# Performance work log

Hardware: AMD Instinct MI355X
Metric: run time of the kernel (lower is better)

Reference implementation:

```python
import jax, jax.numpy as jnp
import numpy as np

N = 100000
K = 4
E = 1600000
EPS = 1e-5


def gcn_conv(x, src, dst, W, b):
    # PyG GCNConv with improved=True: self-loop weight 2, symmetric norm.
    h = x @ W  # [N, out]
    ones = jnp.ones(src.shape, dtype=x.dtype)
    deg = jax.ops.segment_sum(ones, dst, num_segments=N) + 2.0  # improved self-loop adds 2
    dis = jax.lax.rsqrt(deg)
    coef = dis[src] * dis[dst]  # [E]
    agg = jax.ops.segment_sum(h[src] * coef[:, None], dst, num_segments=N)
    agg = agg + (2.0 * dis * dis)[:, None] * h  # self-loop contribution (weight 2)
    return agg + b


def expert_forward(flatten, src, dst, W1, b1, g, bt, W2, b2):
    x = gcn_conv(flatten, src, dst, W1, b1)
    x = jax.nn.relu(x)
    # BatchNorm1d(track_running_stats=False): batch statistics, biased var
    mu = jnp.mean(x, axis=0)
    var = jnp.mean(jnp.square(x - mu), axis=0)
    x = (x - mu) * jax.lax.rsqrt(var + EPS) * g + bt
    return gcn_conv(x, src, dst, W2, b2)  # [N, 2] logits


def setup_inputs() -> dict:
    key = jax.random.key(0)
    ks = jax.random.split(key, 8)
    flatten = jax.random.normal(ks[0], (N, 256), dtype=jnp.float32)
    moe_features = jax.random.normal(ks[1], (N, 256), dtype=jnp.float32)
    edge_index = jax.random.randint(ks[2], (K, 2, E), 0, N, dtype=jnp.int32)
    W1 = jax.random.normal(ks[3], (K, 256, 64), dtype=jnp.float32) * 0.05
    b1 = jnp.zeros((K, 64), dtype=jnp.float32)
    gamma = jnp.ones((K, 64), dtype=jnp.float32)
    beta = jnp.zeros((K, 64), dtype=jnp.float32)
    W2 = jax.random.normal(ks[4], (K, 64, 2), dtype=jnp.float32) * 0.1
    b2 = jnp.zeros((K, 2), dtype=jnp.float32)
    Wg = jax.random.normal(ks[5], (256, K), dtype=jnp.float32) * 0.05
    bg = jnp.zeros((K,), dtype=jnp.float32)
    return {"flatten": flatten, "moe_features": moe_features, "edge_index": edge_index,
            "W1": W1, "b1": b1, "gamma": gamma, "beta": beta, "W2": W2, "b2": b2,
            "Wg": Wg, "bg": bg}


def reference(flatten, moe_features, edge_index, W1, b1, gamma, beta, W2, b2, Wg, bg):
    src = edge_index[:, 0, :]
    dst = edge_index[:, 1, :]
    # run all experts batched via vmap (flatten shared)
    logits = jax.vmap(expert_forward, in_axes=(None, 0, 0, 0, 0, 0, 0, 0, 0))(
        flatten, src, dst, W1, b1, gamma, beta, W2, b2)  # [K, N, 2]
    logp = jax.nn.log_softmax(logits, axis=-1)
    probs = jax.nn.softmax(logits, axis=-1)
    weights = jax.nn.softmax(moe_features @ Wg + bg, axis=1)  # [N, K]
    # results_concat[:, c] = sum_k weights[:, k] * logp[k, :, c]
    results_concat = jnp.einsum('nk,knc->nc', weights, logp)
    results_probs_concat = jnp.einsum('nk,knc->nc', weights, probs)
    return results_concat, results_probs_concat
```

## Files before the change

kernel.cpp:

```cpp
#include <hip/hip_runtime.h>
#include <math.h>

#define NN 100000
#define KEXP 4
#define EE 1600000
#define EPSV 1e-5f
#define BSHIFT 9
#define BSIZE 512
#define NBUCK 196
#define PCHUNK 4096
#define PG ((EE + PCHUNK - 1) / PCHUNK)
#define SLOTS 64
#define STAGECAP 12288

typedef __attribute__((ext_vector_type(8))) short bfrag8;
typedef __attribute__((ext_vector_type(16))) float facc16;

__device__ __forceinline__ unsigned short f2bf(float f) {
    unsigned u = __float_as_uint(f);
    return (unsigned short)((u + 0x7fff + ((u >> 16) & 1)) >> 16);
}
__device__ __forceinline__ float bf_lo(unsigned u) { return __uint_as_float(u << 16); }
__device__ __forceinline__ float bf_hi(unsigned u) { return __uint_as_float(u & 0xffff0000u); }

__global__ __launch_bounds__(256) void hist_pass(const int* __restrict__ edge,
                                                 int* __restrict__ blockhist, int E) {
    int k = blockIdx.y, bx = blockIdx.x;
    const int* dp = edge + (size_t)k * 2 * E + E;
    __shared__ int hist[NBUCK];
    for (int i = threadIdx.x; i < NBUCK; i += 256) hist[i] = 0;
    __syncthreads();
    int cb = bx * PCHUNK, ce = cb + PCHUNK;
    if (ce > E) ce = E;
    for (int e = cb + (int)threadIdx.x; e < ce; e += 256)
        atomicAdd(&hist[dp[e] >> BSHIFT], 1);
    __syncthreads();
    for (int i = threadIdx.x; i < NBUCK; i += 256)
        blockhist[((size_t)k * PG + bx) * NBUCK + i] = hist[i];
}

__global__ __launch_bounds__(256) void scan_pass(int* __restrict__ blockhist,
                                                 int* __restrict__ bbase,
                                                 int* __restrict__ rowptr,
                                                 int n, int E) {
    int k = blockIdx.x;
    int t = threadIdx.x;
    int running = 0;
    if (t < NBUCK) {
        for (int j = 0; j < PG; j++) {
            size_t idx = ((size_t)k * PG + j) * NBUCK + t;
            int v = blockhist[idx];
            blockhist[idx] = running;
            running += v;
        }
    }
    __shared__ int sd[256];
    sd[t] = (t < NBUCK) ? running : 0;
    __syncthreads();
    for (int o = 1; o < 256; o <<= 1) {
        int x = (t >= o) ? sd[t - o] : 0;
        __syncthreads();
        sd[t] += x;
        __syncthreads();
    }
    if (t < NBUCK) bbase[k * (NBUCK + 1) + t] = sd[t] - running;
    if (t == 0) {
        bbase[k * (NBUCK + 1) + NBUCK] = E;
        rowptr[(size_t)k * (n + 1) + n] = E;
    }
}

__global__ __launch_bounds__(256) void partition_pass(const int* __restrict__ edge,
                                                      const int* __restrict__ blockhist,
                                                      const int* __restrict__ bbase,
                                                      unsigned* __restrict__ bstream,
                                                      int E) {
    int k = blockIdx.y, bx = blockIdx.x;
    int t = threadIdx.x;
    __shared__ int hist[NBUCK];
    __shared__ int lofs[NBUCK + 1];
    __shared__ int gbase[NBUCK];
    __shared__ int tmp[256];
    __shared__ unsigned stage[PCHUNK];
    for (int i = t; i < NBUCK; i += 256) {
        hist[i] = 0;
        gbase[i] = bbase[k * (NBUCK + 1) + i] + blockhist[((size_t)k * PG + bx) * NBUCK + i];
    }
    __syncthreads();
    const int* sp = edge + (size_t)k * 2 * E;
    const int* dp = sp + E;
    int cb = bx * PCHUNK, ce = cb + PCHUNK;
    if (ce > E) ce = E;
    int cnt = ce - cb;
    for (int e = cb + t; e < ce; e += 256)
        atomicAdd(&hist[dp[e] >> BSHIFT], 1);
    __syncthreads();
    int v = (t < NBUCK) ? hist[t] : 0;
    tmp[t] = v;
    __syncthreads();
    for (int o = 1; o < 256; o <<= 1) {
        int x = (t >= o) ? tmp[t - o] : 0;
        __syncthreads();
        tmp[t] += x;
        __syncthreads();
    }
    if (t < NBUCK) { lofs[t] = tmp[t] - v; hist[t] = tmp[t] - v; }
    if (t == 0) lofs[NBUCK] = cnt;
    __syncthreads();
    for (int e = cb + t; e < ce; e += 256) {
        int s = sp[e];
        int d = dp[e];
        int r = atomicAdd(&hist[d >> BSHIFT], 1);
        stage[r] = ((unsigned)(d & (BSIZE - 1)) << 17) | (unsigned)s;
    }
    __syncthreads();
    unsigned* bs = bstream + (size_t)k * E;
    for (int i = t; i < cnt; i += 256) {
        int lo = 0, hi = NBUCK;
        while (hi - lo > 1) {
            int mid = (lo + hi) >> 1;
            if (lofs[mid] <= i) lo = mid; else hi = mid;
        }
        bs[gbase[lo] + (i - lofs[lo])] = stage[i];
    }
}

__global__ __launch_bounds__(256) void bucket_build(const int* __restrict__ bbase,
                                                    const unsigned* __restrict__ bstream,
                                                    int* __restrict__ rowptr,
                                                    float* __restrict__ dis,
                                                    int* __restrict__ adj,
                                                    int n, int E) {
    int k = blockIdx.y;
    int b = blockIdx.x;
    int nb = b << BSHIFT;
    int t = threadIdx.x;
    __shared__ int hist[BSIZE];
    __shared__ int curx[BSIZE];
    __shared__ int tmp[256];
    __shared__ int stage[STAGECAP];
    hist[t] = 0;
    hist[t + 256] = 0;
    __syncthreads();
    int beg = bbase[k * (NBUCK + 1) + b];
    int end = bbase[k * (NBUCK + 1) + b + 1];
    int cnt = end - beg;
    const unsigned* bs = bstream + (size_t)k * E;
    for (int p = beg + t; p < end; p += 256) {
        atomicAdd(&hist[bs[p] >> 17], 1);
    }
    __syncthreads();
    int a0 = hist[2 * t], a1 = hist[2 * t + 1];
    tmp[t] = a0 + a1;
    __syncthreads();
    for (int o = 1; o < 256; o <<= 1) {
        int x = (t >= o) ? tmp[t - o] : 0;
        __syncthreads();
        tmp[t] += x;
        __syncthreads();
    }
    int ex = tmp[t] - (a0 + a1);
    int l0 = ex;
    int l1 = ex + a0;
    curx[2 * t] = l0;
    curx[2 * t + 1] = l1;
    int* rp = rowptr + (size_t)k * (n + 1);
    float* dk = dis + (size_t)k * n;
    int node0 = nb + 2 * t, node1 = nb + 2 * t + 1;
    if (node0 < n) { rp[node0] = beg + l0; dk[node0] = rsqrtf((float)a0 + 2.0f); }
    if (node1 < n) { rp[node1] = beg + l1; dk[node1] = rsqrtf((float)a1 + 2.0f); }
    __syncthreads();
    int* aj = adj + (size_t)k * E;
    for (int p = beg + t; p < end; p += 256) {
        unsigned pk = bs[p];
        int pos = atomicAdd(&curx[pk >> 17], 1);
        int sv = (int)(pk & 0x1FFFFu);
        if (pos < STAGECAP) stage[pos] = sv;
        else aj[beg + pos] = sv;
    }
    __syncthreads();
    int lim = cnt < STAGECAP ? cnt : STAGECAP;
    int head = (4 - (beg & 3)) & 3;
    if (head > lim) head = lim;
    if (t < head) aj[beg + t] = stage[t];
    int nv = (lim - head) >> 2;
    for (int i = t; i < nv; i += 256) {
        int s4 = head + 4 * i;
        uint4 v = make_uint4((unsigned)stage[s4], (unsigned)stage[s4 + 1],
                             (unsigned)stage[s4 + 2], (unsigned)stage[s4 + 3]);
        *(uint4*)&aj[beg + s4] = v;
    }
    int tail0 = head + 4 * nv;
    for (int i = tail0 + t; i < lim; i += 256) aj[beg + i] = stage[i];
}

__global__ __launch_bounds__(256) void a2bf_kernel(const float* __restrict__ A,
                                                   unsigned short* __restrict__ abf,
                                                   int n4) {
    int i = blockIdx.x * 256 + threadIdx.x;
    if (i >= n4) return;
    float4 v = ((const float4*)A)[i];
    ushort4 o;
    o.x = f2bf(v.x); o.y = f2bf(v.y); o.z = f2bf(v.z); o.w = f2bf(v.w);
    ((ushort4*)abf)[i] = o;
}

__global__ __launch_bounds__(256) void w2bf_kernel(const float* __restrict__ W1,
                                                   unsigned short* __restrict__ Wt) {
    int k = blockIdx.x;
    for (int idx = threadIdx.x; idx < 64 * 256; idx += 256) {
        int c = idx >> 8;
        int kk = idx & 255;
        Wt[(size_t)k * 64 * 256 + c * 256 + kk] = f2bf(W1[(size_t)k * 256 * 64 + kk * 64 + c]);
    }
}

__global__ __launch_bounds__(256) void gemm1_mfma(
    const unsigned short* __restrict__ abf,
    const unsigned short* __restrict__ Wt,
    const float* __restrict__ dk,
    unsigned short* __restrict__ phbf,
    int M) {
    __shared__ __align__(16) unsigned short As[64][72];
    __shared__ __align__(16) unsigned short Bs[64][72];
    int t = threadIdx.x;
    int row0 = blockIdx.x * 64;
    int wid = t >> 6, lane = t & 63;
    int qr = wid >> 1, qc = wid & 1;
    facc16 acc;
    for (int i = 0; i < 16; i++) acc[i] = 0.f;

    for (int kc = 0; kc < 256; kc += 64) {
        for (int i = 0; i < 2; i++) {
            int fid = t + i * 256;
            int r = fid >> 3;
            int o = (fid & 7) * 8;
            int row = row0 + r;
            uint4 v = make_uint4(0u, 0u, 0u, 0u);
            if (row < M) v = *(const uint4*)&abf[(size_t)row * 256 + kc + o];
            *(uint4*)&As[r][o] = v;
        }
        for (int i = 0; i < 2; i++) {
            int fid = t + i * 256;
            int c = fid >> 3;
            int o = (fid & 7) * 8;
            uint4 v = *(const uint4*)&Wt[(size_t)c * 256 + kc + o];
            *(uint4*)&Bs[c][o] = v;
        }
        __syncthreads();
        int arow = qr * 32 + (lane & 31);
        int bcol = qc * 32 + (lane & 31);
        int ko = (lane >> 5) * 8;
        for (int kk = 0; kk < 64; kk += 16) {
            bfrag8 a = *(const bfrag8*)&As[arow][kk + ko];
            bfrag8 b = *(const bfrag8*)&Bs[bcol][kk + ko];
            acc = __builtin_amdgcn_mfma_f32_32x32x16_bf16(a, b, acc, 0, 0, 0);
        }
        __syncthreads();
    }
    int col = qc * 32 + (lane & 31);
    for (int i = 0; i < 16; i++) {
        int rl = (i & 3) + 8 * (i >> 2) + 4 * (lane >> 5);
        int row = row0 + qr * 32 + rl;
        if (row < M) phbf[(size_t)row * 64 + col] = f2bf(dk[row] * acc[i]);
    }
}

__global__ __launch_bounds__(256) void gemm1_fp32(
    const float* __restrict__ A, const float* __restrict__ W,
    const float* __restrict__ dk,
    unsigned short* __restrict__ phbf, int M) {
    __shared__ __align__(16) float As[64][65];
    __shared__ __align__(16) float Ws[64][68];
    int t = threadIdx.x;
    int row0 = blockIdx.x * 64;
    int tr = t >> 4;
    int tc = t & 15;
    float acc[4][4] = {{0.f}};
    for (int kc = 0; kc < 256; kc += 64) {
        for (int i = 0; i < 4; i++) {
            int fid = t + i * 256;
            int r = fid >> 4;
            int c4 = (fid & 15) << 2;
            int row = row0 + r;
            float4 v = make_float4(0.f, 0.f, 0.f, 0.f);
            if (row < M) v = *(const float4*)&A[(size_t)row * 256 + kc + c4];
            As[r][c4] = v.x; As[r][c4 + 1] = v.y; As[r][c4 + 2] = v.z; As[r][c4 + 3] = v.w;
        }
        for (int i = 0; i < 4; i++) {
            int fid = t + i * 256;
            int r = fid >> 4;
            int c4 = (fid & 15) << 2;
            float4 v = *(const float4*)&W[(size_t)(kc + r) * 64 + c4];
            *(float4*)&Ws[r][c4] = v;
        }
        __syncthreads();
        for (int kk = 0; kk < 64; kk++) {
            float a0 = As[tr * 4 + 0][kk];
            float a1 = As[tr * 4 + 1][kk];
            float a2 = As[tr * 4 + 2][kk];
            float a3 = As[tr * 4 + 3][kk];
            float4 w = *(const float4*)&Ws[kk][tc * 4];
            acc[0][0] += a0 * w.x; acc[0][1] += a0 * w.y; acc[0][2] += a0 * w.z; acc[0][3] += a0 * w.w;
            acc[1][0] += a1 * w.x; acc[1][1] += a1 * w.y; acc[1][2] += a1 * w.z; acc[1][3] += a1 * w.w;
            acc[2][0] += a2 * w.x; acc[2][1] += a2 * w.y; acc[2][2] += a2 * w.z; acc[2][3] += a2 * w.w;
            acc[3][0] += a3 * w.x; acc[3][1] += a3 * w.y; acc[3][2] += a3 * w.z; acc[3][3] += a3 * w.w;
        }
        __syncthreads();
    }
    for (int i = 0; i < 4; i++) {
        int row = row0 + tr * 4 + i;
        if (row >= M) continue;
        float dn = dk[row];
        ushort4 o;
        o.x = f2bf(dn * acc[i][0]); o.y = f2bf(dn * acc[i][1]);
        o.z = f2bf(dn * acc[i][2]); o.w = f2bf(dn * acc[i][3]);
        *(ushort4*)&phbf[(size_t)row * 64 + 4 * tc] = o;
    }
}

__global__ __launch_bounds__(256) void gather1(const int* __restrict__ rowptr,
                                               const int* __restrict__ adj,
                                               const float* __restrict__ dis,
                                               const unsigned short* __restrict__ phbf,
                                               const float* __restrict__ b1,
                                               float* __restrict__ x,
                                               float* __restrict__ accum, int n) {
    __shared__ float ls[4][64];
    __shared__ float lq[4][64];
    ((float*)ls)[threadIdx.x] = 0.f;
    ((float*)lq)[threadIdx.x] = 0.f;
    __syncthreads();
    int w = threadIdx.x >> 6;
    int node = blockIdx.x * 4 + w;
    int lane = threadIdx.x & 63;
    int g = lane >> 4;
    int q = lane & 15;
    if (node < n) {
        int beg = rowptr[node], end = rowptr[node + 1];
        float a0 = 0.f, a1 = 0.f, a2 = 0.f, a3 = 0.f;
        float c0 = 0.f, c1 = 0.f, c2 = 0.f, c3 = 0.f;
        int j = beg;
        for (; j + 8 <= end; j += 8) {
            int s0 = adj[j + g];
            int s1 = adj[j + 4 + g];
            uint2 u0 = *(const uint2*)&phbf[(size_t)s0 * 64 + 4 * q];
            uint2 u1 = *(const uint2*)&phbf[(size_t)s1 * 64 + 4 * q];
            a0 += bf_lo(u0.x); a1 += bf_hi(u0.x);
            a2 += bf_lo(u0.y); a3 += bf_hi(u0.y);
            c0 += bf_lo(u1.x); c1 += bf_hi(u1.x);
            c2 += bf_lo(u1.y); c3 += bf_hi(u1.y);
        }
        for (; j < end; j += 4) {
            int jj = j + g;
            if (jj < end) {
                int s = adj[jj];
                uint2 u = *(const uint2*)&phbf[(size_t)s * 64 + 4 * q];
                a0 += bf_lo(u.x); a1 += bf_hi(u.x);
                a2 += bf_lo(u.y); a3 += bf_hi(u.y);
            }
        }
        a0 += c0; a1 += c1; a2 += c2; a3 += c3;
        a0 += __shfl_xor(a0, 16); a1 += __shfl_xor(a1, 16);
        a2 += __shfl_xor(a2, 16); a3 += __shfl_xor(a3, 16);
        a0 += __shfl_xor(a0, 32); a1 += __shfl_xor(a1, 32);
        a2 += __shfl_xor(a2, 32); a3 += __shfl_xor(a3, 32);
        if (g == 0) {
            float dn = dis[node];
            uint2 us = *(const uint2*)&phbf[(size_t)node * 64 + 4 * q];
            float4 bv = *(const float4*)&b1[4 * q];
            float v0 = dn * (a0 + 2.f * bf_lo(us.x)) + bv.x;
            float v1 = dn * (a1 + 2.f * bf_hi(us.x)) + bv.y;
            float v2 = dn * (a2 + 2.f * bf_lo(us.y)) + bv.z;
            float v3 = dn * (a3 + 2.f * bf_hi(us.y)) + bv.w;
            v0 = fmaxf(v0, 0.f); v1 = fmaxf(v1, 0.f);
            v2 = fmaxf(v2, 0.f); v3 = fmaxf(v3, 0.f);
            *(float4*)&x[(size_t)node * 64 + 4 * q] = make_float4(v0, v1, v2, v3);
            *(float4*)&ls[w][4 * q] = make_float4(v0, v1, v2, v3);
            *(float4*)&lq[w][4 * q] = make_float4(v0 * v0, v1 * v1, v2 * v2, v3 * v3);
        }
    }
    __syncthreads();
    if (threadIdx.x < 64) {
        int c = threadIdx.x;
        float S = ls[0][c] + ls[1][c] + ls[2][c] + ls[3][c];
        float Q = lq[0][c] + lq[1][c] + lq[2][c] + lq[3][c];
        float* slot = accum + (size_t)(blockIdx.x & (SLOTS - 1)) * 128;
        unsafeAtomicAdd(&slot[c], S);
        unsafeAtomicAdd(&slot[64 + c], Q);
    }
}

__global__ __launch_bounds__(256) void bn_gemm2(const float* __restrict__ x,
                                                const float* __restrict__ accum,
                                                const float* __restrict__ g,
                                                const float* __restrict__ bt,
                                                const float* __restrict__ W2,
                                                const float* __restrict__ dk,
                                                float* __restrict__ ph, int M) {
    __shared__ float a_s[64], b_s[64];
    int t = threadIdx.x;
    if (t < 64) {
        float S = 0.f, Q = 0.f;
        for (int s = 0; s < SLOTS; s++) {
            S += accum[(size_t)s * 128 + t];
            Q += accum[(size_t)s * 128 + 64 + t];
        }
        float mu = S / (float)M;
        float var = Q / (float)M - mu * mu;
        float istdg = rsqrtf(var + EPSV) * g[t];
        a_s[t] = istdg;
        b_s[t] = bt[t] - mu * istdg;
    }
    __syncthreads();
    int w = t >> 6;
    int c = t & 63;
    float a = a_s[c], b = b_s[c];
    float w20 = W2[c * 2], w21 = W2[c * 2 + 1];
    for (int node = blockIdx.x * 4 + w; node < M; node += gridDim.x * 4) {
        float v = x[(size_t)node * 64 + c] * a + b;
        float p0 = v * w20;
        float p1 = v * w21;
        for (int off = 32; off; off >>= 1) {
            p0 += __shfl_down(p0, off);
            p1 += __shfl_down(p1, off);
        }
        if (c == 0) {
            float dn = dk[node];
            *(float2*)&ph[(size_t)node * 2] = make_float2(dn * p0, dn * p1);
        }
    }
}

__global__ __launch_bounds__(256) void gather2_all(const int* __restrict__ rowptr,
                                                   const int* __restrict__ adj,
                                                   const float* __restrict__ dis,
                                                   const float* __restrict__ phall,
                                                   const float* __restrict__ b2,
                                                   float* __restrict__ agg2,
                                                   int n, int E) {
    int B = blockIdx.x;
    int k = (B & 7) >> 1;
    int jb = ((B >> 3) << 1) | (B & 1);
    int node = jb * 256 + (int)threadIdx.x;
    if (node >= n) return;
    const int* rp = rowptr + (size_t)k * (n + 1);
    const int* aj = adj + (size_t)k * E;
    const float* ph = phall + (size_t)k * n * 2;
    float dn = dis[(size_t)k * n + node];
    int beg = rp[node], end = rp[node + 1];
    float a0 = 0.f, a1 = 0.f;
    int j = beg;
    for (; j + 2 <= end; j += 2) {
        int s0 = aj[j], s1 = aj[j + 1];
        float2 v0 = *(const float2*)&ph[(size_t)s0 * 2];
        float2 v1 = *(const float2*)&ph[(size_t)s1 * 2];
        a0 += v0.x + v1.x;
        a1 += v0.y + v1.y;
    }
    if (j < end) {
        int s0 = aj[j];
        float2 v0 = *(const float2*)&ph[(size_t)s0 * 2];
        a0 += v0.x;
        a1 += v0.y;
    }
    float2 pn = *(const float2*)&ph[(size_t)node * 2];
    float2 o;
    o.x = dn * (a0 + 2.f * pn.x) + b2[k * 2];
    o.y = dn * (a1 + 2.f * pn.y) + b2[k * 2 + 1];
    *(float2*)&agg2[((size_t)k * n + node) * 2] = o;
}

__global__ __launch_bounds__(256) void gate_kernel(const float* __restrict__ moe,
                                                   const float* __restrict__ Wg,
                                                   const float* __restrict__ bg,
                                                   float* __restrict__ wbuf, int M) {
    int n = (int)((blockIdx.x * (size_t)blockDim.x + threadIdx.x) >> 6);
    int lane = threadIdx.x & 63;
    if (n >= M) return;
    float4 mf = *(const float4*)&moe[(size_t)n * 256 + lane * 4];
    const float* wr = &Wg[lane * 16];
    float a0 = mf.x * wr[0] + mf.y * wr[4] + mf.z * wr[8] + mf.w * wr[12];
    float a1 = mf.x * wr[1] + mf.y * wr[5] + mf.z * wr[9] + mf.w * wr[13];
    float a2 = mf.x * wr[2] + mf.y * wr[6] + mf.z * wr[10] + mf.w * wr[14];
    float a3 = mf.x * wr[3] + mf.y * wr[7] + mf.z * wr[11] + mf.w * wr[15];
    for (int mask = 1; mask < 64; mask <<= 1) {
        a0 += __shfl_xor(a0, mask);
        a1 += __shfl_xor(a1, mask);
        a2 += __shfl_xor(a2, mask);
        a3 += __shfl_xor(a3, mask);
    }
    if (lane == 0) {
        float g0 = a0 + bg[0], g1 = a1 + bg[1], g2 = a2 + bg[2], g3 = a3 + bg[3];
        float m = fmaxf(fmaxf(g0, g1), fmaxf(g2, g3));
        float w0 = expf(g0 - m), w1 = expf(g1 - m), w2 = expf(g2 - m), w3 = expf(g3 - m);
        float inv = 1.f / (w0 + w1 + w2 + w3);
        *(float4*)&wbuf[(size_t)n * 4] =
            make_float4(w0 * inv, w1 * inv, w2 * inv, w3 * inv);
    }
}

__global__ __launch_bounds__(256) void mix_kernel(const float* __restrict__ wbuf,
                                                  const float* __restrict__ agg2,
                                                  float* __restrict__ out, int M) {
    int n = blockIdx.x * 256 + threadIdx.x;
    if (n >= M) return;
    float4 wv = *(const float4*)&wbuf[(size_t)n * 4];
    float wk[4] = {wv.x, wv.y, wv.z, wv.w};
    float o0 = 0.f, o1 = 0.f, q0 = 0.f, q1 = 0.f;
    for (int kk = 0; kk < 4; kk++) {
        float2 l = *(const float2*)&agg2[((size_t)kk * M + n) * 2];
        float mm = fmaxf(l.x, l.y);
        float lse = mm + logf(expf(l.x - mm) + expf(l.y - mm));
        float lp0 = l.x - lse, lp1 = l.y - lse;
        o0 += wk[kk] * lp0; o1 += wk[kk] * lp1;
        q0 += wk[kk] * expf(lp0); q1 += wk[kk] * expf(lp1);
    }
    *(float2*)&out[(size_t)n * 2] = make_float2(o0, o1);
    *(float2*)&out[(size_t)2 * M + n * 2] = make_float2(q0, q1);
}

extern "C" void kernel_launch(void* const* d_in, const int* in_sizes, int n_in,
                              void* d_out, int out_size, void* d_ws, size_t ws_size,
                              hipStream_t stream) {
    const float* flatten = (const float*)d_in[0];
    const float* moe     = (const float*)d_in[1];
    const int*   edge    = (const int*)d_in[2];
    const float* W1      = (const float*)d_in[3];
    const float* b1      = (const float*)d_in[4];
    const float* gamma   = (const float*)d_in[5];
    const float* beta    = (const float*)d_in[6];
    const float* W2      = (const float*)d_in[7];
    const float* b2      = (const float*)d_in[8];
    const float* Wg      = (const float*)d_in[9];
    const float* bg      = (const float*)d_in[10];
    float* out = (float*)d_out;

    const int N = NN, E = EE, K = KEXP;

    char* ws = (char*)d_ws;
    size_t off = 0;
    auto alloc = [&](size_t bytes) -> void* {
        void* p = (void*)(ws + off);
        off += (bytes + 255) & ~(size_t)255;
        return p;
    };
    int*   rowptr    = (int*)alloc((size_t)K * (N + 1) * 4);
    float* dis       = (float*)alloc((size_t)K * N * 4);
    int*   blockhist = (int*)alloc((size_t)K * PG * NBUCK * 4);
    int*   bbase     = (int*)alloc((size_t)K * (NBUCK + 1) * 4);
    int*   adj       = (int*)alloc((size_t)K * E * 4);
    unsigned short* hbf = (unsigned short*)alloc((size_t)N * 64 * 2);
    float* x         = (float*)alloc((size_t)N * 64 * 4);
    float* h2all     = (float*)alloc((size_t)K * N * 2 * 4);
    float* agg2      = (float*)alloc((size_t)K * N * 2 * 4);
    float* accum     = (float*)alloc((size_t)K * SLOTS * 128 * 4);
    float* wbuf      = (float*)alloc((size_t)N * 4 * 4);
    size_t base_need = off;
    unsigned short* abf = (unsigned short*)alloc((size_t)N * 256 * 2);
    unsigned short* Wt  = (unsigned short*)alloc((size_t)K * 64 * 256 * 2);
    size_t mfma_need = off;
    (void)in_sizes; (void)n_in; (void)out_size; (void)base_need;
    bool use_mfma = (ws_size >= mfma_need);

    unsigned* bstream = (unsigned*)hbf;

    hipMemsetAsync(accum, 0, (size_t)K * SLOTS * 128 * 4, stream);
    hist_pass<<<dim3(PG, K), 256, 0, stream>>>(edge, blockhist, E);
    scan_pass<<<K, 256, 0, stream>>>(blockhist, bbase, rowptr, N, E);
    partition_pass<<<dim3(PG, K), 256, 0, stream>>>(edge, blockhist, bbase, bstream, E);
    bucket_build<<<dim3(NBUCK, K), 256, 0, stream>>>(bbase, bstream, rowptr, dis, adj, N, E);

    if (use_mfma) {
        a2bf_kernel<<<(N * 256 / 4 + 255) / 256, 256, 0, stream>>>(flatten, abf, N * 256 / 4);
        w2bf_kernel<<<K, 256, 0, stream>>>(W1, Wt);
    }

    gate_kernel<<<(int)(((size_t)N * 64 + 255) / 256), 256, 0, stream>>>(
        moe, Wg, bg, wbuf, N);

    for (int k = 0; k < K; k++) {
        const int* rp = rowptr + (size_t)k * (N + 1);
        const int* aj = adj + (size_t)k * E;
        const float* dk = dis + (size_t)k * N;
        float* ak = accum + (size_t)k * SLOTS * 128;
        if (use_mfma) {
            gemm1_mfma<<<(N + 63) / 64, 256, 0, stream>>>(
                abf, Wt + (size_t)k * 64 * 256, dk, hbf, N);
        } else {
            gemm1_fp32<<<(N + 63) / 64, 256, 0, stream>>>(
                flatten, W1 + (size_t)k * 256 * 64, dk, hbf, N);
        }
        gather1<<<(N + 3) / 4, 256, 0, stream>>>(
            rp, aj, dk, hbf, b1 + (size_t)k * 64, x, ak, N);
        bn_gemm2<<<1024, 256, 0, stream>>>(
            x, ak, gamma + (size_t)k * 64, beta + (size_t)k * 64,
            W2 + (size_t)k * 128, dk, h2all + (size_t)k * N * 2, N);
    }
    gather2_all<<<1568, 256, 0, stream>>>(
        rowptr, adj, dis, h2all, b2, agg2, N, E);
    mix_kernel<<<(N + 255) / 256, 256, 0, stream>>>(wbuf, agg2, out, N);
}
```

Measured before the change: 834.9 us.

## Batch all experts into single launches per stage and rework gate kernel

When the workspace is large enough, all four experts now run together: the per-expert loop of three launches each is replaced by one GEMM1, one gather1 and one BN+GEMM2 launch that cover every expert via the grid y dimension or an index decode that interleaves experts across blocks. This removes launch gaps and lets the per-expert stages fill the GPU concurrently, at the cost of K-fold larger intermediate buffers (bf16 h and fp32 x for all experts). The gate kernel also changes from one wavefront per row with shuffle reductions to one thread per row, with Wg staged in shared memory. The old sequential path is kept as a fallback when the workspace is small.

```diff
diff --git a/kernel.cpp b/kernel.cpp
--- a/kernel.cpp
+++ b/kernel.cpp
@@ -215,12 +215,16 @@
     }
 }
 
-__global__ __launch_bounds__(256) void gemm1_mfma(
+__global__ __launch_bounds__(256) void gemm1_mfma_all(
     const unsigned short* __restrict__ abf,
-    const unsigned short* __restrict__ Wt,
-    const float* __restrict__ dk,
-    unsigned short* __restrict__ phbf,
+    const unsigned short* __restrict__ Wtall,
+    const float* __restrict__ dis,
+    unsigned short* __restrict__ phall,
     int M) {
+    int k = blockIdx.y;
+    const unsigned short* Wt = Wtall + (size_t)k * 64 * 256;
+    const float* dk = dis + (size_t)k * M;
+    unsigned short* phbf = phall + (size_t)k * M * 64;
     __shared__ __align__(16) unsigned short As[64][72];
     __shared__ __align__(16) unsigned short Bs[64][72];
     int t = threadIdx.x;
@@ -266,10 +270,14 @@
     }
 }
 
-__global__ __launch_bounds__(256) void gemm1_fp32(
-    const float* __restrict__ A, const float* __restrict__ W,
-    const float* __restrict__ dk,
-    unsigned short* __restrict__ phbf, int M) {
+__global__ __launch_bounds__(256) void gemm1_fp32_all(
+    const float* __restrict__ A, const float* __restrict__ W1,
+    const float* __restrict__ dis,
+    unsigned short* __restrict__ phall, int M) {
+    int k = blockIdx.y;
+    const float* W = W1 + (size_t)k * 256 * 64;
+    const float* dk = dis + (size_t)k * M;
+    unsigned short* phbf = phall + (size_t)k * M * 64;
     __shared__ __align__(16) float As[64][65];
     __shared__ __align__(16) float Ws[64][68];
     int t = threadIdx.x;
@@ -319,31 +327,47 @@
     }
 }
 
-__global__ __launch_bounds__(256) void gather1(const int* __restrict__ rowptr,
-                                               const int* __restrict__ adj,
-                                               const float* __restrict__ dis,
-                                               const unsigned short* __restrict__ phbf,
-                                               const float* __restrict__ b1,
-                                               float* __restrict__ x,
-                                               float* __restrict__ accum, int n) {
+__global__ __launch_bounds__(256) void gather1_all(const int* __restrict__ rowptr,
+                                                   const int* __restrict__ adj,
+                                                   const float* __restrict__ dis,
+                                                   const unsigned short* __restrict__ phall,
+                                                   const float* __restrict__ b1all,
+                                                   float* __restrict__ xall,
+                                                   float* __restrict__ accum,
+                                                   int n, int E, int merged) {
+    int B = blockIdx.x;
+    int k, nb4;
+    if (merged) {
+        k = (B >> 1) & 3;
+        nb4 = (((B >> 3) << 1) | (B & 1));
+    } else {
+        k = 0;
+        nb4 = B;
+    }
+    const int* rp = rowptr + (size_t)k * (n + 1);
+    const int* aj = adj + (size_t)k * E;
+    const unsigned short* phbf = phall + (size_t)k * n * 64;
+    const float* b1 = b1all + (size_t)k * 64;
+    float* x = xall + (size_t)k * n * 64;
+
     __shared__ float ls[4][64];
     __shared__ float lq[4][64];
     ((float*)ls)[threadIdx.x] = 0.f;
     ((float*)lq)[threadIdx.x] = 0.f;
     __syncthreads();
     int w = threadIdx.x >> 6;
-    int node = blockIdx.x * 4 + w;
+    int node = nb4 * 4 + w;
     int lane = threadIdx.x & 63;
     int g = lane >> 4;
     int q = lane & 15;
     if (node < n) {
-        int beg = rowptr[node], end = rowptr[node + 1];
+        int beg = rp[node], end = rp[node + 1];
         float a0 = 0.f, a1 = 0.f, a2 = 0.f, a3 = 0.f;
         float c0 = 0.f, c1 = 0.f, c2 = 0.f, c3 = 0.f;
         int j = beg;
         for (; j + 8 <= end; j += 8) {
-            int s0 = adj[j + g];
-            int s1 = adj[j + 4 + g];
+            int s0 = aj[j + g];
+            int s1 = aj[j + 4 + g];
             uint2 u0 = *(const uint2*)&phbf[(size_t)s0 * 64 + 4 * q];
             uint2 u1 = *(const uint2*)&phbf[(size_t)s1 * 64 + 4 * q];
             a0 += bf_lo(u0.x); a1 += bf_hi(u0.x);
@@ -354,7 +378,7 @@
         for (; j < end; j += 4) {
             int jj = j + g;
             if (jj < end) {
-                int s = adj[jj];
+                int s = aj[jj];
                 uint2 u = *(const uint2*)&phbf[(size_t)s * 64 + 4 * q];
                 a0 += bf_lo(u.x); a1 += bf_hi(u.x);
                 a2 += bf_lo(u.y); a3 += bf_hi(u.y);
@@ -366,7 +390,7 @@
         a0 += __shfl_xor(a0, 32); a1 += __shfl_xor(a1, 32);
         a2 += __shfl_xor(a2, 32); a3 += __shfl_xor(a3, 32);
         if (g == 0) {
-            float dn = dis[node];
+            float dn = dis[(size_t)k * n + node];
             uint2 us = *(const uint2*)&phbf[(size_t)node * 64 + 4 * q];
             float4 bv = *(const float4*)&b1[4 * q];
             float v0 = dn * (a0 + 2.f * bf_lo(us.x)) + bv.x;
@@ -385,26 +409,34 @@
         int c = threadIdx.x;
         float S = ls[0][c] + ls[1][c] + ls[2][c] + ls[3][c];
         float Q = lq[0][c] + lq[1][c] + lq[2][c] + lq[3][c];
-        float* slot = accum + (size_t)(blockIdx.x & (SLOTS - 1)) * 128;
+        float* slot = accum + (size_t)k * SLOTS * 128 + (size_t)(nb4 & (SLOTS - 1)) * 128;
         unsafeAtomicAdd(&slot[c], S);
         unsafeAtomicAdd(&slot[64 + c], Q);
     }
 }
 
-__global__ __launch_bounds__(256) void bn_gemm2(const float* __restrict__ x,
-                                                const float* __restrict__ accum,
-                                                const float* __restrict__ g,
-                                                const float* __restrict__ bt,
-                                                const float* __restrict__ W2,
-                                                const float* __restrict__ dk,
-                                                float* __restrict__ ph, int M) {
+__global__ __launch_bounds__(256) void bn_gemm2_all(const float* __restrict__ xall,
+                                                    const float* __restrict__ accum,
+                                                    const float* __restrict__ gall,
+                                                    const float* __restrict__ btall,
+                                                    const float* __restrict__ W2all,
+                                                    const float* __restrict__ dis,
+                                                    float* __restrict__ h2all, int M) {
+    int k = blockIdx.y;
+    const float* x = xall + (size_t)k * M * 64;
+    const float* acb = accum + (size_t)k * SLOTS * 128;
+    const float* g = gall + (size_t)k * 64;
+    const float* bt = btall + (size_t)k * 64;
+    const float* W2 = W2all + (size_t)k * 128;
+    const float* dk = dis + (size_t)k * M;
+    float* ph = h2all + (size_t)k * M * 2;
     __shared__ float a_s[64], b_s[64];
     int t = threadIdx.x;
     if (t < 64) {
         float S = 0.f, Q = 0.f;
         for (int s = 0; s < SLOTS; s++) {
-            S += accum[(size_t)s * 128 + t];
-            Q += accum[(size_t)s * 128 + 64 + t];
+            S += acb[(size_t)s * 128 + t];
+            Q += acb[(size_t)s * 128 + 64 + t];
         }
         float mu = S / (float)M;
         float var = Q / (float)M - mu * mu;
@@ -475,29 +507,27 @@
                                                    const float* __restrict__ Wg,
                                                    const float* __restrict__ bg,
                                                    float* __restrict__ wbuf, int M) {
-    int n = (int)((blockIdx.x * (size_t)blockDim.x + threadIdx.x) >> 6);
-    int lane = threadIdx.x & 63;
+    __shared__ float wg_s[1024];
+    for (int i = threadIdx.x; i < 1024; i += 256) wg_s[i] = Wg[i];
+    __syncthreads();
+    int n = blockIdx.x * 256 + threadIdx.x;
     if (n >= M) return;
-    float4 mf = *(const float4*)&moe[(size_t)n * 256 + lane * 4];
-    const float* wr = &Wg[lane * 16];
-    float a0 = mf.x * wr[0] + mf.y * wr[4] + mf.z * wr[8] + mf.w * wr[12];
-    float a1 = mf.x * wr[1] + mf.y * wr[5] + mf.z * wr[9] + mf.w * wr[13];
-    float a2 = mf.x * wr[2] + mf.y * wr[6] + mf.z * wr[10] + mf.w * wr[14];
-    float a3 = mf.x * wr[3] + mf.y * wr[7] + mf.z * wr[11] + mf.w * wr[15];
-    for (int mask = 1; mask < 64; mask <<= 1) {
-        a0 += __shfl_xor(a0, mask);
-        a1 += __shfl_xor(a1, mask);
-        a2 += __shfl_xor(a2, mask);
-        a3 += __shfl_xor(a3, mask);
-    }
-    if (lane == 0) {
-        float g0 = a0 + bg[0], g1 = a1 + bg[1], g2 = a2 + bg[2], g3 = a3 + bg[3];
-        float m = fmaxf(fmaxf(g0, g1), fmaxf(g2, g3));
-        float w0 = expf(g0 - m), w1 = expf(g1 - m), w2 = expf(g2 - m), w3 = expf(g3 - m);
-        float inv = 1.f / (w0 + w1 + w2 + w3);
-        *(float4*)&wbuf[(size_t)n * 4] =
-            make_float4(w0 * inv, w1 * inv, w2 * inv, w3 * inv);
-    }
+    const float4* row = (const float4*)&moe[(size_t)n * 256];
+    float a0 = 0.f, a1 = 0.f, a2 = 0.f, a3 = 0.f;
+    #pragma unroll 8
+    for (int j = 0; j < 64; j++) {
+        float4 v = row[j];
+        const float* wj = &wg_s[j * 16];
+        a0 += v.x * wj[0] + v.y * wj[4] + v.z * wj[8]  + v.w * wj[12];
+        a1 += v.x * wj[1] + v.y * wj[5] + v.z * wj[9]  + v.w * wj[13];
+        a2 += v.x * wj[2] + v.y * wj[6] + v.z * wj[10] + v.w * wj[14];
+        a3 += v.x * wj[3] + v.y * wj[7] + v.z * wj[11] + v.w * wj[15];
+    }
+    float g0 = a0 + bg[0], g1 = a1 + bg[1], g2 = a2 + bg[2], g3 = a3 + bg[3];
+    float m = fmaxf(fmaxf(g0, g1), fmaxf(g2, g3));
+    float w0 = expf(g0 - m), w1 = expf(g1 - m), w2 = expf(g2 - m), w3 = expf(g3 - m);
+    float inv = 1.f / (w0 + w1 + w2 + w3);
+    *(float4*)&wbuf[(size_t)n * 4] = make_float4(w0 * inv, w1 * inv, w2 * inv, w3 * inv);
 }
 
 __global__ __launch_bounds__(256) void mix_kernel(const float* __restrict__ wbuf,
@@ -550,20 +580,29 @@
     int*   blockhist = (int*)alloc((size_t)K * PG * NBUCK * 4);
     int*   bbase     = (int*)alloc((size_t)K * (NBUCK + 1) * 4);
     int*   adj       = (int*)alloc((size_t)K * E * 4);
-    unsigned short* hbf = (unsigned short*)alloc((size_t)N * 64 * 2);
-    float* x         = (float*)alloc((size_t)N * 64 * 4);
     float* h2all     = (float*)alloc((size_t)K * N * 2 * 4);
     float* agg2      = (float*)alloc((size_t)K * N * 2 * 4);
     float* accum     = (float*)alloc((size_t)K * SLOTS * 128 * 4);
     float* wbuf      = (float*)alloc((size_t)N * 4 * 4);
-    size_t base_need = off;
-    unsigned short* abf = (unsigned short*)alloc((size_t)N * 256 * 2);
-    unsigned short* Wt  = (unsigned short*)alloc((size_t)K * 64 * 256 * 2);
-    size_t mfma_need = off;
-    (void)in_sizes; (void)n_in; (void)out_size; (void)base_need;
-    bool use_mfma = (ws_size >= mfma_need);
-
-    unsigned* bstream = (unsigned*)hbf;
+    unsigned short* Wt = (unsigned short*)alloc((size_t)K * 64 * 256 * 2);
+    size_t common_end = off;
+
+    unsigned short* phallA = (unsigned short*)alloc((size_t)K * N * 64 * 2);
+    float* xallA = (float*)alloc((size_t)K * N * 64 * 4);
+    size_t merged_need = off;
+
+    off = common_end;
+    unsigned short* hbfB = (unsigned short*)alloc((size_t)N * 64 * 2);
+    float* xB = (float*)alloc((size_t)N * 64 * 4);
+    size_t fb_base_need = off;
+    unsigned short* abfB = (unsigned short*)alloc((size_t)N * 256 * 2);
+    size_t fb_mfma_need = off;
+    (void)in_sizes; (void)n_in; (void)out_size; (void)fb_base_need;
+
+    bool merged = (ws_size >= merged_need);
+    bool fb_mfma = (ws_size >= fb_mfma_need);
+
+    unsigned* bstream = merged ? (unsigned*)phallA : (unsigned*)hbfB;
 
     hipMemsetAsync(accum, 0, (size_t)K * SLOTS * 128 * 4, stream);
     hist_pass<<<dim3(PG, K), 256, 0, stream>>>(edge, blockhist, E);
@@ -571,31 +610,40 @@
     partition_pass<<<dim3(PG, K), 256, 0, stream>>>(edge, blockhist, bbase, bstream, E);
     bucket_build<<<dim3(NBUCK, K), 256, 0, stream>>>(bbase, bstream, rowptr, dis, adj, N, E);
 
-    if (use_mfma) {
+    gate_kernel<<<(N + 255) / 256, 256, 0, stream>>>(moe, Wg, bg, wbuf, N);
+
+    if (merged) {
+        unsigned short* abf = (unsigned short*)xallA;
         a2bf_kernel<<<(N * 256 / 4 + 255) / 256, 256, 0, stream>>>(flatten, abf, N * 256 / 4);
         w2bf_kernel<<<K, 256, 0, stream>>>(W1, Wt);
-    }
-
-    gate_kernel<<<(int)(((size_t)N * 64 + 255) / 256), 256, 0, stream>>>(
-        moe, Wg, bg, wbuf, N);
-
-    for (int k = 0; k < K; k++) {
-        const int* rp = rowptr + (size_t)k * (N + 1);
-        const int* aj = adj + (size_t)k * E;
-        const float* dk = dis + (size_t)k * N;
-        float* ak = accum + (size_t)k * SLOTS * 128;
-        if (use_mfma) {
-            gemm1_mfma<<<(N + 63) / 64, 256, 0, stream>>>(
-                abf, Wt + (size_t)k * 64 * 256, dk, hbf, N);
-        } else {
-            gemm1_fp32<<<(N + 63) / 64, 256, 0, stream>>>(
-                flatten, W1 + (size_t)k * 256 * 64, dk, hbf, N);
-        }
-        gather1<<<(N + 3) / 4, 256, 0, stream>>>(
-            rp, aj, dk, hbf, b1 + (size_t)k * 64, x, ak, N);
-        bn_gemm2<<<1024, 256, 0, stream>>>(
-            x, ak, gamma + (size_t)k * 64, beta + (size_t)k * 64,
-            W2 + (size_t)k * 128, dk, h2all + (size_t)k * N * 2, N);
+        gemm1_mfma_all<<<dim3((N + 63) / 64, K), 256, 0, stream>>>(
+            abf, Wt, dis, phallA, N);
+        gather1_all<<<N, 256, 0, stream>>>(
+            rowptr, adj, dis, phallA, b1, xallA, accum, N, E, 1);
+        bn_gemm2_all<<<dim3(1024, K), 256, 0, stream>>>(
+            xallA, accum, gamma, beta, W2, dis, h2all, N);
+    } else {
+        if (fb_mfma) {
+            a2bf_kernel<<<(N * 256 / 4 + 255) / 256, 256, 0, stream>>>(flatten, abfB, N * 256 / 4);
+            w2bf_kernel<<<K, 256, 0, stream>>>(W1, Wt);
+        }
+        for (int k = 0; k < K; k++) {
+            if (fb_mfma) {
+                gemm1_mfma_all<<<dim3((N + 63) / 64, 1), 256, 0, stream>>>(
+                    abfB, Wt + (size_t)k * 64 * 256, dis + (size_t)k * N, hbfB, N);
+            } else {
+                gemm1_fp32_all<<<dim3((N + 63) / 64, 1), 256, 0, stream>>>(
+                    flatten, W1 + (size_t)k * 256 * 64, dis + (size_t)k * N, hbfB, N);
+            }
+            gather1_all<<<(N + 3) / 4, 256, 0, stream>>>(
+                rowptr + (size_t)k * (N + 1), adj + (size_t)k * E,
+                dis + (size_t)k * N, hbfB, b1 + (size_t)k * 64, xB,
+                accum + (size_t)k * SLOTS * 128, N, E, 0);
+            bn_gemm2_all<<<dim3(1024, 1), 256, 0, stream>>>(
+                xB, accum + (size_t)k * SLOTS * 128, gamma + (size_t)k * 64,
+                beta + (size_t)k * 64, W2 + (size_t)k * 128,
+                dis + (size_t)k * N, h2all + (size_t)k * N * 2, N);
+        }
     }
     gather2_all<<<1568, 256, 0, stream>>>(
         rowptr, adj, dis, h2all, b2, agg2, N, E);
```

After: 789.6 us. 1.06x faster.
